# Optimization experiments

Measured on AMD Instinct MI355X. Metric: run time of the kernel, lower is better.

Reference implementation:

```python
import jax, jax.numpy as jnp
import numpy as np

DIM = 512
HEADS = 8
DIM_HEAD = 64
INNER = HEADS * DIM_HEAD  # 512
SCALE = DIM_HEAD ** -0.5
LN_EPS = 1e-5


def setup_inputs() -> dict:
    key = jax.random.key(0)
    k1, k2, k3, k4 = jax.random.split(key, 4)
    b, p, n = 4, 64, 256
    x = jax.random.normal(k1, (b, p, n, DIM), dtype=jnp.float32)
    ln_g = jnp.ones((DIM,), jnp.float32)
    ln_b = jnp.zeros((DIM,), jnp.float32)
    # stored as [in, out] for x @ W
    w_qkv = jax.random.normal(k2, (DIM, 3 * INNER), jnp.float32) * (DIM ** -0.5)
    w_out = jax.random.normal(k3, (INNER, DIM), jnp.float32) * (INNER ** -0.5)
    b_out = jnp.zeros((DIM,), jnp.float32)
    return {"x": x, "ln_g": ln_g, "ln_b": ln_b, "w_qkv": w_qkv,
            "w_out": w_out, "b_out": b_out}


def reference(x, ln_g, ln_b, w_qkv, w_out, b_out):
    b, p, n, _ = x.shape
    # LayerNorm over last dim
    mu = jnp.mean(x, axis=-1, keepdims=True)
    var = jnp.mean(jnp.square(x - mu), axis=-1, keepdims=True)
    xn = (x - mu) * jax.lax.rsqrt(var + LN_EPS) * ln_g + ln_b
    # QKV projection (no bias)
    qkv = xn @ w_qkv                                   # [b,p,n,3*INNER]
    q, k, v = jnp.split(qkv, 3, axis=-1)
    def to_heads(t):
        return t.reshape(b, p, n, HEADS, DIM_HEAD).transpose(0, 1, 3, 2, 4)
    q, k, v = to_heads(q), to_heads(k), to_heads(v)    # [b,p,h,n,d]
    dots = jnp.einsum('bphnd,bphmd->bphnm', q, k) * SCALE
    attn = jax.nn.softmax(dots, axis=-1)
    out = jnp.einsum('bphnm,bphmd->bphnd', attn, v)    # [b,p,h,n,d]
    out = out.transpose(0, 1, 3, 2, 4).reshape(b, p, n, INNER)
    return out @ w_out + b_out
```

## Files before the change

kernel.cpp:

```cpp
#include <hip/hip_runtime.h>
#include <stdint.h>

#define DIMD 512
#define HEADS 8
#define DHEAD 64
#define NSEQ 256
#define NGRP 256
#define TRIPLE 1536
#define ATT_SCALE 0.125f

typedef float f32x4 __attribute__((ext_vector_type(4)));
typedef _Float16 half8 __attribute__((ext_vector_type(8)));
typedef _Float16 half4 __attribute__((ext_vector_type(4)));

#define GLD16(gp, lp) __builtin_amdgcn_global_load_lds( \
    (const __attribute__((address_space(1))) void*)(gp), \
    (__attribute__((address_space(3))) void*)(lp), 16, 0, 0)
#define BAR() __builtin_amdgcn_s_barrier()
#define VMW(n) asm volatile("s_waitcnt vmcnt(" #n ")" ::: "memory")

__global__ __launch_bounds__(256) void k_pre(const float* __restrict__ x,
                                             const float* __restrict__ g,
                                             const float* __restrict__ b,
                                             const float* __restrict__ wq,
                                             const float* __restrict__ wo,
                                             _Float16* __restrict__ xn,
                                             _Float16* __restrict__ wtq,
                                             _Float16* __restrict__ wto) {
  int bid = blockIdx.x;
  if (bid < 256) {
    __shared__ float T[64][65];
    const float* src; _Float16* dst; int spitch, ti, tj;
    if (bid < 192) { src = wq; dst = wtq; spitch = TRIPLE; ti = bid / 24; tj = bid % 24; }
    else { int t = bid - 192; src = wo; dst = wto; spitch = DIMD; ti = t >> 3; tj = t & 7; }
#pragma unroll
    for (int it = 0; it < 4; ++it) {
      int idx = it * 256 + threadIdx.x;
      int rr = idx >> 4, c4 = (idx & 15) * 4;
      *(f32x4*)&T[rr][c4] = *(const f32x4*)&src[(size_t)(ti * 64 + rr) * spitch + tj * 64 + c4];
    }
    __syncthreads();
#pragma unroll
    for (int it = 0; it < 2; ++it) {
      int idx = it * 256 + threadIdx.x;
      int rr2 = idx >> 3, c8 = (idx & 7) * 8;
      half8 o;
#pragma unroll
      for (int j = 0; j < 8; ++j) o[j] = (_Float16)T[c8 + j][rr2];
      *(half8*)&dst[(size_t)(tj * 64 + rr2) * DIMD + ti * 64 + c8] = o;
    }
    return;
  }
  int row = (bid - 256) * 4 + (threadIdx.x >> 6);
  int lane = threadIdx.x & 63;
  const float* xr = x + (size_t)row * DIMD + lane * 8;
  float v[8];
  *(f32x4*)(v)     = *(const f32x4*)(xr);
  *(f32x4*)(v + 4) = *(const f32x4*)(xr + 4);
  float s = 0.f, ss = 0.f;
#pragma unroll
  for (int j = 0; j < 8; ++j) { s += v[j]; ss += v[j] * v[j]; }
#pragma unroll
  for (int m = 1; m < 64; m <<= 1) { s += __shfl_xor(s, m); ss += __shfl_xor(ss, m); }
  float mean = s * (1.f / DIMD);
  float var  = ss * (1.f / DIMD) - mean * mean;
  float rstd = rsqrtf(var + 1e-5f);
  const float* gp = g + lane * 8;
  const float* bp = b + lane * 8;
  half8 o;
#pragma unroll
  for (int j = 0; j < 8; ++j) o[j] = (_Float16)((v[j] - mean) * rstd * gp[j] + bp[j]);
  *(half8*)(xn + (size_t)row * DIMD + lane * 8) = o;
}

template <int N, int LDA, bool F32OUT>
__global__ __launch_bounds__(512, 2) void k_gemm8(const _Float16* __restrict__ A,
                                                  const _Float16* __restrict__ BT,
                                                  _Float16* __restrict__ Ch,
                                                  float* __restrict__ Cf,
                                                  const float* __restrict__ bias) {
  constexpr int NT = N / 256;
  constexpr int NWG = 256 * NT;
  constexpr int CPX = NWG / 8;
  int bb_ = blockIdx.x;
  int logical = (bb_ & 7) * CPX + (bb_ >> 3);
  int mt = logical / NT, nt = logical % NT;
  int m0 = mt * 256, n0 = nt * 256;

  int tid = threadIdx.x, lane = tid & 63, w = tid >> 6;
  int wrow = w >> 2, wcol = w & 3;
  int l15 = lane & 15, lg = lane >> 4;
  const int sr = lane >> 3;
  const int ss = lane & 7;

  __shared__ _Float16 S[65536];

  f32x4 acc[8][4] = {};
  half8 af0[4][2], af1[4][2], bf0[2][2], bf1[2][2];

  auto stageA = [&](int d, int kt, int hf) {
#pragma unroll
    for (int cc = 0; cc < 2; ++cc) {
      int rbase = cc * 128 + hf * 64 + w * 8;
      const _Float16* gp = A + (size_t)(m0 + rbase + sr) * LDA + kt * 64 + (ss ^ sr) * 8;
      GLD16(gp, &S[d * 32768 + rbase * 64]);
    }
  };
  auto stageB = [&](int d, int kt, int hf) {
#pragma unroll
    for (int cc = 0; cc < 2; ++cc) {
      int i = cc * 64 + w * 8;
      int rbase = (i >> 5) * 64 + hf * 32 + (i & 31);
      const _Float16* gp = BT + (size_t)(n0 + rbase + sr) * 512 + kt * 64 + (ss ^ sr) * 8;
      GLD16(gp, &S[d * 32768 + 16384 + rbase * 64]);
    }
  };
  auto loadA = [&](int c, int mh, half8 (&af)[4][2]) {
#pragma unroll
    for (int mf = 0; mf < 4; ++mf) {
      int row = wrow * 128 + mh * 64 + mf * 16 + l15;
#pragma unroll
      for (int kk = 0; kk < 2; ++kk) {
        int byte = row * 128 + ((kk * 64 + lg * 16) ^ ((row & 7) << 4));
        af[mf][kk] = *(const half8*)((const char*)&S[c * 32768] + byte);
      }
    }
  };
  auto loadB = [&](int c, int nh, half8 (&bf)[2][2]) {
#pragma unroll
    for (int nf = 0; nf < 2; ++nf) {
      int row = wcol * 64 + nh * 32 + nf * 16 + l15;
#pragma unroll
      for (int kk = 0; kk < 2; ++kk) {
        int byte = row * 128 + ((kk * 64 + lg * 16) ^ ((row & 7) << 4));
        bf[nf][kk] = *(const half8*)((const char*)&S[c * 32768 + 16384] + byte);
      }
    }
  };
  auto quad = [&](int mh, int nh, half8 (&af)[4][2], half8 (&bf)[2][2]) {
    __builtin_amdgcn_s_setprio(1);
#pragma unroll
    for (int mf = 0; mf < 4; ++mf)
#pragma unroll
      for (int nf = 0; nf < 2; ++nf)
#pragma unroll
        for (int kk = 0; kk < 2; ++kk)
          acc[mh * 4 + mf][nh * 2 + nf] = __builtin_amdgcn_mfma_f32_16x16x32_f16(
              af[mf][kk], bf[nf][kk], acc[mh * 4 + mf][nh * 2 + nf], 0, 0, 0);
    __builtin_amdgcn_s_setprio(0);
  };

  stageA(0, 0, 0); stageB(0, 0, 0); stageB(0, 0, 1); stageA(0, 0, 1);
  VMW(4); BAR();

#pragma unroll
  for (int t = 0; t < 8; ++t) {
    const int c = t & 1, d = c ^ 1;
    loadA(c, 0, af0); loadB(c, 0, bf0);
    if (t > 0) quad(1, 1, af1, bf1);
    if (t < 7) { stageA(d, t + 1, 0); VMW(4); } else { VMW(2); }
    BAR();
    loadB(c, 1, bf1);
    quad(0, 0, af0, bf0);
    if (t < 7) { stageB(d, t + 1, 0); VMW(4); } else { VMW(0); }
    BAR();
    loadA(c, 1, af1);
    quad(0, 1, af0, bf1);
    if (t < 7) stageB(d, t + 1, 1);
    BAR();
    quad(1, 0, af1, bf0);
    if (t < 7) { stageA(d, t + 1, 1); VMW(4); }
    BAR();
  }
  quad(1, 1, af1, bf1);

  float bbv[4];
  if constexpr (F32OUT) {
#pragma unroll
    for (int nq = 0; nq < 4; ++nq)
      bbv[nq] = bias[n0 + wcol * 64 + (nq >> 1) * 32 + (nq & 1) * 16 + l15];
  }
#pragma unroll
  for (int mq = 0; mq < 8; ++mq)
#pragma unroll
    for (int nq = 0; nq < 4; ++nq)
#pragma unroll
      for (int r = 0; r < 4; ++r) {
        int row = m0 + wrow * 128 + (mq >> 2) * 64 + (mq & 3) * 16 + lg * 4 + r;
        int col = n0 + wcol * 64 + (nq >> 1) * 32 + (nq & 1) * 16 + l15;
        if constexpr (F32OUT)
          Cf[(size_t)row * N + col] = acc[mq][nq][r] + bbv[nq];
        else
          Ch[(size_t)row * N + col] = (_Float16)acc[mq][nq][r];
      }
}

__global__ __launch_bounds__(256, 2) void k_attn(_Float16* __restrict__ qkv) {
  int g = blockIdx.x >> 3, h = blockIdx.x & 7;
  int tid = threadIdx.x, lane = tid & 63, w = tid >> 6;
  int l15 = lane & 15, lg = lane >> 4;
  __shared__ _Float16 Kt[64 * 64];
  __shared__ _Float16 Vt[64 * 72];
  __shared__ _Float16 Pl[4][64 * 72];
  const size_t base = (size_t)g * NSEQ * TRIPLE;

  half8 qf[4][2];
#pragma unroll
  for (int nq = 0; nq < 4; ++nq)
#pragma unroll
    for (int kd = 0; kd < 2; ++kd)
      qf[nq][kd] = *(const half8*)&qkv[base + (size_t)(w * 64 + nq * 16 + l15) * TRIPLE
                                       + h * 64 + kd * 32 + lg * 8];

  f32x4 oacc[4][4] = {};
  float mrun[4], lrun[4];
#pragma unroll
  for (int nq = 0; nq < 4; ++nq) { mrun[nq] = -3.0e38f; lrun[nq] = 0.f; }

  const int srow = lane >> 3;
  const int sslot = lane & 7;

  for (int kt = 0; kt < 4; ++kt) {
    __syncthreads();
#pragma unroll
    for (int rnd = 0; rnd < 2; ++rnd) {
      int rbase = rnd * 32 + w * 8;
      const _Float16* gp = &qkv[base + (size_t)(kt * 64 + rbase + srow) * TRIPLE
                                + 512 + h * 64 + (sslot ^ srow) * 8];
      GLD16(gp, &Kt[rbase * 64]);
    }
#pragma unroll
    for (int i = 0; i < 2; ++i) {
      int idx = tid + i * 256;
      int key = idx >> 3, dh0 = (idx & 7) * 8;
      half8 vv = *(const half8*)&qkv[base + (size_t)(kt * 64 + key) * TRIPLE + 1024 + h * 64 + dh0];
#pragma unroll
      for (int j = 0; j < 8; ++j) Vt[(dh0 + j) * 72 + key] = vv[j];
    }
    VMW(0);
    __syncthreads();

    f32x4 st[4][4] = {};
#pragma unroll
    for (int kd = 0; kd < 2; ++kd) {
      half8 kf[4];
#pragma unroll
      for (int mk = 0; mk < 4; ++mk) {
        int r = mk * 16 + l15;
        int byte = r * 128 + ((kd * 64 + lg * 16) ^ ((r & 7) << 4));
        kf[mk] = *(const half8*)((const char*)Kt + byte);
      }
#pragma unroll
      for (int mk = 0; mk < 4; ++mk)
#pragma unroll
        for (int nq = 0; nq < 4; ++nq)
          st[mk][nq] = __builtin_amdgcn_mfma_f32_16x16x32_f16(kf[mk], qf[nq][kd], st[mk][nq], 0, 0, 0);
    }

    float alpha[4];
#pragma unroll
    for (int nq = 0; nq < 4; ++nq) {
      float pm = -3.0e38f;
#pragma unroll
      for (int mk = 0; mk < 4; ++mk)
#pragma unroll
        for (int r = 0; r < 4; ++r) {
          st[mk][nq][r] *= ATT_SCALE;
          pm = fmaxf(pm, st[mk][nq][r]);
        }
      pm = fmaxf(pm, __shfl_xor(pm, 16));
      pm = fmaxf(pm, __shfl_xor(pm, 32));
      float mn = fmaxf(mrun[nq], pm);
      alpha[nq] = __expf(mrun[nq] - mn);
      mrun[nq] = mn;
      float ps = 0.f;
#pragma unroll
      for (int mk = 0; mk < 4; ++mk) {
        half4 p4;
#pragma unroll
        for (int r = 0; r < 4; ++r) {
          float e = __expf(st[mk][nq][r] - mn);
          ps += e;
          p4[r] = (_Float16)e;
        }
        *(half4*)&Pl[w][(nq * 16 + l15) * 72 + mk * 16 + lg * 4] = p4;
      }
      ps += __shfl_xor(ps, 16);
      ps += __shfl_xor(ps, 32);
      lrun[nq] = lrun[nq] * alpha[nq] + ps;
    }

#pragma unroll
    for (int mp = 0; mp < 4; ++mp)
#pragma unroll
      for (int r = 0; r < 4; ++r) {
        float av = __shfl(alpha[mp], lg * 4 + r);
#pragma unroll
        for (int nd = 0; nd < 4; ++nd) oacc[mp][nd][r] *= av;
      }

    __syncthreads();

#pragma unroll
    for (int kp = 0; kp < 2; ++kp) {
      int co = kp * 32 + lg * 8;
      half8 pf[4], vf[4];
#pragma unroll
      for (int mp = 0; mp < 4; ++mp) pf[mp] = *(const half8*)&Pl[w][(mp * 16 + l15) * 72 + co];
#pragma unroll
      for (int nd = 0; nd < 4; ++nd) vf[nd] = *(const half8*)&Vt[(nd * 16 + l15) * 72 + co];
#pragma unroll
      for (int mp = 0; mp < 4; ++mp)
#pragma unroll
        for (int nd = 0; nd < 4; ++nd)
          oacc[mp][nd] = __builtin_amdgcn_mfma_f32_16x16x32_f16(pf[mp], vf[nd], oacc[mp][nd], 0, 0, 0);
    }
  }

#pragma unroll
  for (int mp = 0; mp < 4; ++mp)
#pragma unroll
    for (int r = 0; r < 4; ++r) {
      float li = 1.f / __shfl(lrun[mp], lg * 4 + r);
      int q = w * 64 + mp * 16 + lg * 4 + r;
#pragma unroll
      for (int nd = 0; nd < 4; ++nd)
        qkv[base + (size_t)q * TRIPLE + h * 64 + nd * 16 + l15] =
            (_Float16)(oacc[mp][nd][r] * li);
    }
}

extern "C" void kernel_launch(void* const* d_in, const int* in_sizes, int n_in,
                              void* d_out, int out_size, void* d_ws, size_t ws_size,
                              hipStream_t stream) {
  const float* x     = (const float*)d_in[0];
  const float* ln_g  = (const float*)d_in[1];
  const float* ln_b  = (const float*)d_in[2];
  const float* w_qkv = (const float*)d_in[3];
  const float* w_out = (const float*)d_in[4];
  const float* b_out = (const float*)d_in[5];

  char* ws = (char*)d_ws;
  _Float16* qkv = (_Float16*)ws;
  _Float16* wtq = (_Float16*)(ws + 201326592ull);
  _Float16* wto = (_Float16*)(ws + 201326592ull + 1572864ull);
  _Float16* xn  = (_Float16*)d_out;
  float* out    = (float*)d_out;

  k_pre<<<16640, 256, 0, stream>>>(x, ln_g, ln_b, w_qkv, w_out, xn, wtq, wto);
  k_gemm8<TRIPLE, DIMD, false><<<1536, 512, 0, stream>>>(xn, wtq, qkv, nullptr, nullptr);
  k_attn<<<2048, 256, 0, stream>>>(qkv);
  k_gemm8<DIMD, TRIPLE, true><<<512, 512, 0, stream>>>(qkv, wto, nullptr, out, b_out);
}
```

Before: 278.8 us.

## Double-buffer K/V tiles in attention and stage GEMM epilogue through LDS

The attention kernel now double-buffers the K and V tiles in shared memory. It issues the next tile's K async load and V register load before computing the current tile, which overlaps global loads with the MFMA work. The mid-loop full block barrier is replaced by an lgkmcnt wait, since each wave only reads its own P buffer. Separately, the GEMM epilogue writes accumulators into swizzled shared memory and then stores coalesced 16-byte vectors to global memory instead of scattered scalar stores. The cost is more LDS use in attention, which may reduce occupancy, plus extra barriers in the epilogue.

```diff
diff --git a/kernel.cpp b/kernel.cpp
--- a/kernel.cpp
+++ b/kernel.cpp
@@ -18,6 +18,7 @@
     (__attribute__((address_space(3))) void*)(lp), 16, 0, 0)
 #define BAR() __builtin_amdgcn_s_barrier()
 #define VMW(n) asm volatile("s_waitcnt vmcnt(" #n ")" ::: "memory")
+#define LGKM0() asm volatile("s_waitcnt lgkmcnt(0)" ::: "memory")
 
 __global__ __launch_bounds__(256) void k_pre(const float* __restrict__ x,
                                              const float* __restrict__ g,
@@ -174,71 +175,120 @@
   }
   quad(1, 1, af1, bf1);
 
-  float bbv[4];
-  if constexpr (F32OUT) {
+  char* Sb = (char*)S;
+  if constexpr (!F32OUT) {
+    __syncthreads();
+#pragma unroll
+    for (int mq = 0; mq < 8; ++mq)
+#pragma unroll
+      for (int nq = 0; nq < 4; ++nq)
+#pragma unroll
+        for (int r = 0; r < 4; ++r) {
+          int row = wrow * 128 + (mq >> 2) * 64 + (mq & 3) * 16 + lg * 4 + r;
+          int col = wcol * 64 + (nq >> 1) * 32 + (nq & 1) * 16 + l15;
+          *(_Float16*)(Sb + row * 512 + ((col * 2) ^ ((row & 7) << 4))) =
+              (_Float16)acc[mq][nq][r];
+        }
+    __syncthreads();
+#pragma unroll
+    for (int it = 0; it < 16; ++it) {
+      int idx = it * 512 + tid;
+      int row = idx >> 5, ch = idx & 31;
+      half8 vv = *(const half8*)(Sb + row * 512 + ((ch * 16) ^ ((row & 7) << 4)));
+      *(half8*)&Ch[(size_t)(m0 + row) * N + n0 + ch * 8] = vv;
+    }
+  } else {
+    float bbv[4];
 #pragma unroll
     for (int nq = 0; nq < 4; ++nq)
       bbv[nq] = bias[n0 + wcol * 64 + (nq >> 1) * 32 + (nq & 1) * 16 + l15];
+    __syncthreads();
+#pragma unroll
+    for (int hh = 0; hh < 2; ++hh) {
+      if (hh) { LGKM0(); BAR(); }
+#pragma unroll
+      for (int m2 = 0; m2 < 4; ++m2)
+#pragma unroll
+        for (int nq = 0; nq < 4; ++nq)
+#pragma unroll
+          for (int r = 0; r < 4; ++r) {
+            int packed = wrow * 64 + m2 * 16 + lg * 4 + r;
+            int col = wcol * 64 + (nq >> 1) * 32 + (nq & 1) * 16 + l15;
+            *(float*)(Sb + packed * 1024 + ((col * 4) ^ ((packed & 7) << 4))) =
+                acc[hh * 4 + m2][nq][r] + bbv[nq];
+          }
+      LGKM0(); BAR();
+#pragma unroll
+      for (int it = 0; it < 16; ++it) {
+        int idx = it * 512 + tid;
+        int prow = idx >> 6, ch = idx & 63;
+        f32x4 vv = *(const f32x4*)(Sb + prow * 1024 + ((ch * 16) ^ ((prow & 7) << 4)));
+        int row = (prow >> 6) * 128 + hh * 64 + (prow & 63);
+        *(f32x4*)&Cf[(size_t)(m0 + row) * N + n0 + ch * 4] = vv;
+      }
+    }
   }
-#pragma unroll
-  for (int mq = 0; mq < 8; ++mq)
-#pragma unroll
-    for (int nq = 0; nq < 4; ++nq)
-#pragma unroll
-      for (int r = 0; r < 4; ++r) {
-        int row = m0 + wrow * 128 + (mq >> 2) * 64 + (mq & 3) * 16 + lg * 4 + r;
-        int col = n0 + wcol * 64 + (nq >> 1) * 32 + (nq & 1) * 16 + l15;
-        if constexpr (F32OUT)
-          Cf[(size_t)row * N + col] = acc[mq][nq][r] + bbv[nq];
-        else
-          Ch[(size_t)row * N + col] = (_Float16)acc[mq][nq][r];
-      }
 }
 
 __global__ __launch_bounds__(256, 2) void k_attn(_Float16* __restrict__ qkv) {
   int g = blockIdx.x >> 3, h = blockIdx.x & 7;
   int tid = threadIdx.x, lane = tid & 63, w = tid >> 6;
   int l15 = lane & 15, lg = lane >> 4;
-  __shared__ _Float16 Kt[64 * 64];
-  __shared__ _Float16 Vt[64 * 72];
+  __shared__ _Float16 Kt[2][64 * 64];
+  __shared__ _Float16 Vt[2][64 * 72];
   __shared__ _Float16 Pl[4][64 * 72];
   const size_t base = (size_t)g * NSEQ * TRIPLE;
-
-  half8 qf[4][2];
-#pragma unroll
-  for (int nq = 0; nq < 4; ++nq)
-#pragma unroll
-    for (int kd = 0; kd < 2; ++kd)
-      qf[nq][kd] = *(const half8*)&qkv[base + (size_t)(w * 64 + nq * 16 + l15) * TRIPLE
-                                       + h * 64 + kd * 32 + lg * 8];
-
-  f32x4 oacc[4][4] = {};
-  float mrun[4], lrun[4];
-#pragma unroll
-  for (int nq = 0; nq < 4; ++nq) { mrun[nq] = -3.0e38f; lrun[nq] = 0.f; }
-
-  const int srow = lane >> 3;
-  const int sslot = lane & 7;
-
-  for (int kt = 0; kt < 4; ++kt) {
-    __syncthreads();
+  const int srow = lane >> 3, sslot = lane & 7;
+
+  half8 vr[2];
+  auto vload = [&](int kt) {
+#pragma unroll
+    for (int i = 0; i < 2; ++i) {
+      int idx = tid + i * 256;
+      int key = idx >> 3, dh0 = (idx & 7) * 8;
+      vr[i] = *(const half8*)&qkv[base + (size_t)(kt * 64 + key) * TRIPLE + 1024 + h * 64 + dh0];
+    }
+  };
+  auto kstage = [&](int dbuf, int kt) {
 #pragma unroll
     for (int rnd = 0; rnd < 2; ++rnd) {
       int rbase = rnd * 32 + w * 8;
       const _Float16* gp = &qkv[base + (size_t)(kt * 64 + rbase + srow) * TRIPLE
                                 + 512 + h * 64 + (sslot ^ srow) * 8];
-      GLD16(gp, &Kt[rbase * 64]);
-    }
+      GLD16(gp, &Kt[dbuf][rbase * 64]);
+    }
+  };
+  auto vwrite = [&](int dbuf) {
 #pragma unroll
     for (int i = 0; i < 2; ++i) {
       int idx = tid + i * 256;
       int key = idx >> 3, dh0 = (idx & 7) * 8;
-      half8 vv = *(const half8*)&qkv[base + (size_t)(kt * 64 + key) * TRIPLE + 1024 + h * 64 + dh0];
-#pragma unroll
-      for (int j = 0; j < 8; ++j) Vt[(dh0 + j) * 72 + key] = vv[j];
-    }
-    VMW(0);
-    __syncthreads();
+#pragma unroll
+      for (int j = 0; j < 8; ++j) Vt[dbuf][(dh0 + j) * 72 + key] = vr[i][j];
+    }
+  };
+
+  half8 qf[4][2];
+#pragma unroll
+  for (int nq = 0; nq < 4; ++nq)
+#pragma unroll
+    for (int kd = 0; kd < 2; ++kd)
+      qf[nq][kd] = *(const half8*)&qkv[base + (size_t)(w * 64 + nq * 16 + l15) * TRIPLE
+                                       + h * 64 + kd * 32 + lg * 8];
+
+  f32x4 oacc[4][4] = {};
+  float mrun[4], lrun[4];
+#pragma unroll
+  for (int nq = 0; nq < 4; ++nq) { mrun[nq] = -3.0e38f; lrun[nq] = 0.f; }
+
+  kstage(0, 0); vload(0);
+  VMW(0);
+  vwrite(0);
+  LGKM0(); BAR();
+
+  for (int kt = 0; kt < 4; ++kt) {
+    const int c = kt & 1, d = c ^ 1;
+    if (kt < 3) { kstage(d, kt + 1); vload(kt + 1); }
 
     f32x4 st[4][4] = {};
 #pragma unroll
@@ -248,7 +298,7 @@
       for (int mk = 0; mk < 4; ++mk) {
         int r = mk * 16 + l15;
         int byte = r * 128 + ((kd * 64 + lg * 16) ^ ((r & 7) << 4));
-        kf[mk] = *(const half8*)((const char*)Kt + byte);
+        kf[mk] = *(const half8*)((const char*)Kt[c] + byte);
       }
 #pragma unroll
       for (int mk = 0; mk < 4; ++mk)
@@ -299,7 +349,8 @@
         for (int nd = 0; nd < 4; ++nd) oacc[mp][nd][r] *= av;
       }
 
-    __syncthreads();
+    LGKM0();
+    __builtin_amdgcn_sched_barrier(0);
 
 #pragma unroll
     for (int kp = 0; kp < 2; ++kp) {
@@ -308,13 +359,16 @@
 #pragma unroll
       for (int mp = 0; mp < 4; ++mp) pf[mp] = *(const half8*)&Pl[w][(mp * 16 + l15) * 72 + co];
 #pragma unroll
-      for (int nd = 0; nd < 4; ++nd) vf[nd] = *(const half8*)&Vt[(nd * 16 + l15) * 72 + co];
+      for (int nd = 0; nd < 4; ++nd) vf[nd] = *(const half8*)&Vt[c][(nd * 16 + l15) * 72 + co];
 #pragma unroll
       for (int mp = 0; mp < 4; ++mp)
 #pragma unroll
         for (int nd = 0; nd < 4; ++nd)
           oacc[mp][nd] = __builtin_amdgcn_mfma_f32_16x16x32_f16(pf[mp], vf[nd], oacc[mp][nd], 0, 0, 0);
     }
+
+    if (kt < 3) { VMW(0); vwrite(d); }
+    LGKM0(); BAR();
   }
 
 #pragma unroll
```

Result: no change. 281.1 us (+0.8%).
